# Performance work log

Hardware: AMD Instinct MI355X
Metric: run time of the kernel (lower is better)

The kernel has to match this reference:

```python
import jax, jax.numpy as jnp
import numpy as np

B, TD, TE, H = 8, 128, 256, 512


def setup_inputs() -> dict:
    key = jax.random.key(0)
    k1, k2, k3, k4, k5, k6 = jax.random.split(key, 6)
    enc = jax.random.normal(k1, (B, TE, H), dtype=jnp.float32)
    dec = jax.random.normal(k2, (B, TD, H), dtype=jnp.float32)
    mask = jax.random.randint(k3, (B, TE), 0, 2).astype(jnp.bool_)
    # glorot-ish scale for weights
    W1 = jax.random.normal(k4, (H, H), dtype=jnp.float32) * (1.0 / np.sqrt(H))
    W2 = jax.random.normal(k5, (H, H), dtype=jnp.float32) * (1.0 / np.sqrt(H))
    V = jax.random.normal(k6, (H, 1), dtype=jnp.float32) * (1.0 / np.sqrt(H))
    return {"encoder_outputs": enc, "decoder_outputs": dec,
            "encoder_mask": mask, "W1": W1, "W2": W2, "V": V}


def reference(encoder_outputs, decoder_outputs, encoder_mask, W1, W2, V):
    # Bahdanau additive attention.
    # enc: [B, Te, H], dec: [B, Td, H], mask: [B, Te]
    ew = jnp.einsum('bsh,hk->bsk', encoder_outputs, W1)   # [B, Te, H]
    dw = jnp.einsum('bth,hk->btk', decoder_outputs, W2)   # [B, Td, H]
    # broadcast add -> [B, Td, Te, H] (the large intermediate)
    s = jnp.tanh(ew[:, None, :, :] + dw[:, :, None, :])
    score = jnp.einsum('btsh,h->bts', s, V[:, 0])          # [B, Td, Te]
    m = encoder_mask.astype(jnp.float32)                   # [B, Te]
    score = score + (1.0 - m)[:, None, :] * (-1e9)
    attention_weights = jax.nn.softmax(score, axis=2)      # [B, Td, Te]
    context_vector = jnp.einsum('bts,bsh->bth', attention_weights, encoder_outputs)
    return context_vector, attention_weights
```

## Files before the change

kernel.cpp:

```cpp
#include <hip/hip_runtime.h>
#include <hip/hip_bf16.h>
#include <math.h>

constexpr int kB  = 8;
constexpr int kTD = 128;
constexpr int kTE = 256;
constexpr int kH  = 512;

constexpr float kTwoLog2e = 2.8853900817779268f;
constexpr float kLog2e    = 1.4426950408889634f;

constexpr int TM = 4;
constexpr int GEMM_BLOCKS = 384;

typedef __attribute__((ext_vector_type(8)))  short short8;
typedef __attribute__((ext_vector_type(16))) float f32x16;

__device__ __forceinline__ unsigned short f2bf(float x) {
    unsigned int u = __float_as_uint(x);
    return (unsigned short)((u + 0x7fffu + ((u >> 16) & 1u)) >> 16);
}
__device__ __forceinline__ float bf2f(unsigned short h) {
    return __uint_as_float(((unsigned int)h) << 16);
}

__global__ __launch_bounds__(256)
void prep_kernel(const float* __restrict__ enc, const float* __restrict__ dec,
                 const float* __restrict__ W1, const float* __restrict__ W2,
                 const void* __restrict__ mask_raw,
                 float* __restrict__ ewt, float* __restrict__ dwc,
                 float* __restrict__ mask_f) {
    const int bx = blockIdx.x;
    const int tid = threadIdx.x;

    if (bx == GEMM_BLOCKS) {
        const unsigned int* w = (const unsigned int*)mask_raw;
        unsigned int gt1 = 0, flt = 0;
        for (int i = tid; i < 512; i += 256) {
            unsigned int v = w[i];
            if (v == 0x3f800000u) flt = 1;
            else if (v > 1u) gt1 = 1;
        }
        __shared__ unsigned int s_gt1, s_flt;
        if (tid == 0) { s_gt1 = 0u; s_flt = 0u; }
        __syncthreads();
        if (gt1) atomicOr(&s_gt1, 1u);
        if (flt) atomicOr(&s_flt, 1u);
        __syncthreads();
        const int mode = s_flt ? 2 : (s_gt1 ? 1 : 0);
        for (int i = tid; i < kB * kTE; i += 256) {
            float val;
            if (mode == 2)      val = ((const float*)mask_raw)[i];
            else if (mode == 1) val = (float)(((const unsigned char*)mask_raw)[i]);
            else                val = (float)(((const int*)mask_raw)[i]);
            mask_f[i] = val;
        }
        return;
    }

    const int mt = bx >> 3;
    const int nt = bx & 7;
    const bool is_enc = (mt < 32);
    const int m0 = mt * 64;
    const int n0 = nt * 64;
    const float* Abase = is_enc ? (enc + (size_t)m0 * kH)
                                : (dec + (size_t)(m0 - 2048) * kH);
    const float* W = is_enc ? W1 : W2;

    __shared__ __align__(16) unsigned short Ahi[64][40], Alo[64][40];
    __shared__ __align__(16) unsigned short Bhi[64][40], Blo[64][40];
    __shared__ float Ws[32][68];

    const int lane = tid & 63;
    const int wv   = tid >> 6;
    const int wr   = wv >> 1, wc = wv & 1;
    const int col  = lane & 31, hi5 = lane >> 5;

    const int ar  = tid >> 2;
    const int akc = (tid & 3) * 8;
    const int wkr = tid >> 3;
    const int wnc = (tid & 7) * 8;
    const int pn  = tid & 63;
    const int pkc = (tid >> 6) * 8;

    f32x16 acc = {};

    float4 a0p = *(const float4*)&Abase[(size_t)ar * kH + akc];
    float4 a1p = *(const float4*)&Abase[(size_t)ar * kH + akc + 4];
    float4 w0p = *(const float4*)&W[(size_t)wkr * kH + n0 + wnc];
    float4 w1p = *(const float4*)&W[(size_t)wkr * kH + n0 + wnc + 4];

    for (int step = 0; step < 16; ++step) {
        *(float4*)&Ws[wkr][wnc]     = w0p;
        *(float4*)&Ws[wkr][wnc + 4] = w1p;
        {
            uint4 H, L;
            float f[8] = {a0p.x, a0p.y, a0p.z, a0p.w, a1p.x, a1p.y, a1p.z, a1p.w};
            unsigned short hs[8], ls[8];
            #pragma unroll
            for (int j = 0; j < 8; ++j) {
                hs[j] = f2bf(f[j]);
                ls[j] = f2bf(f[j] - bf2f(hs[j]));
            }
            H.x = hs[0] | (hs[1] << 16); H.y = hs[2] | (hs[3] << 16);
            H.z = hs[4] | (hs[5] << 16); H.w = hs[6] | (hs[7] << 16);
            L.x = ls[0] | (ls[1] << 16); L.y = ls[2] | (ls[3] << 16);
            L.z = ls[4] | (ls[5] << 16); L.w = ls[6] | (ls[7] << 16);
            *(uint4*)&Ahi[ar][akc] = H;
            *(uint4*)&Alo[ar][akc] = L;
        }
        __syncthreads();

        {
            uint4 H, L;
            unsigned short hs[8], ls[8];
            #pragma unroll
            for (int j = 0; j < 8; ++j) {
                float x = Ws[pkc + j][pn];
                hs[j] = f2bf(x);
                ls[j] = f2bf(x - bf2f(hs[j]));
            }
            H.x = hs[0] | (hs[1] << 16); H.y = hs[2] | (hs[3] << 16);
            H.z = hs[4] | (hs[5] << 16); H.w = hs[6] | (hs[7] << 16);
            L.x = ls[0] | (ls[1] << 16); L.y = ls[2] | (ls[3] << 16);
            L.z = ls[4] | (ls[5] << 16); L.w = ls[6] | (ls[7] << 16);
            *(uint4*)&Bhi[pn][pkc] = H;
            *(uint4*)&Blo[pn][pkc] = L;
        }

        if (step < 15) {
            const int k1 = (step + 1) * 32;
            a0p = *(const float4*)&Abase[(size_t)ar * kH + k1 + akc];
            a1p = *(const float4*)&Abase[(size_t)ar * kH + k1 + akc + 4];
            w0p = *(const float4*)&W[(size_t)(k1 + wkr) * kH + n0 + wnc];
            w1p = *(const float4*)&W[(size_t)(k1 + wkr) * kH + n0 + wnc + 4];
        }
        __syncthreads();

        #pragma unroll
        for (int kc = 0; kc < 32; kc += 16) {
            const int ka = kc + hi5 * 8;
            short8 ah = *(const short8*)&Ahi[wr * 32 + col][ka];
            short8 al = *(const short8*)&Alo[wr * 32 + col][ka];
            short8 bh = *(const short8*)&Bhi[wc * 32 + col][ka];
            short8 bl = *(const short8*)&Blo[wc * 32 + col][ka];
            acc = __builtin_amdgcn_mfma_f32_32x32x16_bf16(ah, bh, acc, 0, 0, 0);
            acc = __builtin_amdgcn_mfma_f32_32x32x16_bf16(ah, bl, acc, 0, 0, 0);
            acc = __builtin_amdgcn_mfma_f32_32x32x16_bf16(al, bh, acc, 0, 0, 0);
        }
        __syncthreads();
    }

    const int h = n0 + wc * 32 + col;
    if (is_enc) {
        #pragma unroll
        for (int reg = 0; reg < 16; ++reg) {
            const int row = (reg & 3) + 8 * (reg >> 2) + 4 * hi5;
            const int gm = m0 + wr * 32 + row;
            const int bb = gm >> 8, sE = gm & 255;
            float val = __builtin_amdgcn_exp2f(acc[reg] * kTwoLog2e);
            ewt[(((size_t)bb * 128 + (h >> 2)) * 256 + sE) * 4 + (h & 3)] = val;
        }
    } else {
        #pragma unroll
        for (int reg = 0; reg < 16; ++reg) {
            const int row = (reg & 3) + 8 * (reg >> 2) + 4 * hi5;
            const int dm = (m0 - 2048) + wr * 32 + row;
            float val = __builtin_amdgcn_exp2f(acc[reg] * kTwoLog2e);
            dwc[(size_t)dm * kH + h] = val;
        }
    }
}

__global__ __launch_bounds__(1024, 4)
void fused_attn_kernel(const float* __restrict__ ewt, const float* __restrict__ dwc,
                       const float* __restrict__ enc, const float* __restrict__ V,
                       const float* __restrict__ mask_f,
                       float* __restrict__ ctx_out, float* __restrict__ attn_out) {
    const int bid = blockIdx.x;
    const int b   = bid & 7;
    const int t0  = (bid >> 3) * TM;
    const int tid = threadIdx.x;
    const int s   = tid & 255;
    const int hq  = tid >> 8;
    const int hqu = __builtin_amdgcn_readfirstlane(hq);

    __shared__ float p_s[TM * kH];
    __shared__ float v_s[kH];
    __shared__ union {
        float  part[3 * TM * kTE];
        float4 pctx[4][TM][128];
    } u;
    __shared__ float4 wgt4[kTE];
    __shared__ float red_mx[4][TM], red_sm[4][TM];

    if (tid < 512)
        ((float4*)p_s)[tid] =
            ((const float4*)(dwc + (size_t)(b * kTD + t0) * kH))[tid];
    else if (tid < 640)
        ((float4*)v_s)[tid - 512] = ((const float4*)V)[tid - 512];
    __syncthreads();

    const float4* E4 = (const float4*)ewt + ((size_t)(b * 128 + hqu * 32) * 256 + s);
    const float4* Pq = (const float4*)p_s + hqu * 32;
    const float4* Vq = (const float4*)v_s + hqu * 32;

    float a0 = 0.0f, a1 = 0.0f, a2 = 0.0f, a3 = 0.0f;

#define SCORE_T(eV, gg, qoff, accv)                                        \
    {   float4 q = Pq[(qoff) + (gg)];                                      \
        float A_ = fmaf(eV.x, q.x, 1.0f), B_ = fmaf(eV.y, q.y, 1.0f);      \
        float C_ = fmaf(eV.z, q.z, 1.0f), D_ = fmaf(eV.w, q.w, 1.0f);      \
        float t1 = fmaf(vv.y, A_, vv.x * B_);                              \
        float t2 = fmaf(vv.w, C_, vv.z * D_);                              \
        float AB = A_ * B_, CD = C_ * D_;                                  \
        float num = fmaf(t2, AB, t1 * CD);                                 \
        accv = fmaf(num, __builtin_amdgcn_rcpf(AB * CD), accv); }
#define SCORE_STEP(eV, gg)                                                 \
    {   float4 vv = Vq[gg];                                                \
        SCORE_T(eV, gg, 0, a0)   SCORE_T(eV, gg, 128, a1)                  \
        SCORE_T(eV, gg, 256, a2) SCORE_T(eV, gg, 384, a3) }

    float4 e0 = E4[0];
    float4 e1 = E4[256];
    #pragma unroll 4
    for (int g = 0; g < 32; ++g) {
        const int gp = (g + 2 < 32) ? (g + 2) : 31;
        float4 en = E4[(size_t)gp * 256];
        SCORE_STEP(e0, g)
        e0 = e1; e1 = en;
    }
#undef SCORE_STEP
#undef SCORE_T

    if (hq > 0) {
        float* pp = &u.part[(hq - 1) * TM * kTE];
        pp[0 * kTE + s] = a0; pp[1 * kTE + s] = a1;
        pp[2 * kTE + s] = a2; pp[3 * kTE + s] = a3;
    }
    __syncthreads();

    const bool active = (hq == 0);
    const int wvq = s >> 6;
    float sc0, sc1, sc2, sc3;
    if (active) {
        const float* P = u.part;
        const float pen = (1.0f - mask_f[b * kTE + s]) * -1e9f;
        sc0 = -2.0f * ((a0 + P[0 * TM * kTE + 0 * kTE + s]) +
                       (P[1 * TM * kTE + 0 * kTE + s] + P[2 * TM * kTE + 0 * kTE + s])) + pen;
        sc1 = -2.0f * ((a1 + P[0 * TM * kTE + 1 * kTE + s]) +
                       (P[1 * TM * kTE + 1 * kTE + s] + P[2 * TM * kTE + 1 * kTE + s])) + pen;
        sc2 = -2.0f * ((a2 + P[0 * TM * kTE + 2 * kTE + s]) +
                       (P[1 * TM * kTE + 2 * kTE + s] + P[2 * TM * kTE + 2 * kTE + s])) + pen;
        sc3 = -2.0f * ((a3 + P[0 * TM * kTE + 3 * kTE + s]) +
                       (P[1 * TM * kTE + 3 * kTE + s] + P[2 * TM * kTE + 3 * kTE + s])) + pen;
        float m0 = sc0, m1 = sc1, m2 = sc2, m3 = sc3;
        #pragma unroll
        for (int off = 1; off < 64; off <<= 1) {
            m0 = fmaxf(m0, __shfl_xor(m0, off));
            m1 = fmaxf(m1, __shfl_xor(m1, off));
            m2 = fmaxf(m2, __shfl_xor(m2, off));
            m3 = fmaxf(m3, __shfl_xor(m3, off));
        }
        if ((s & 63) == 0) {
            red_mx[wvq][0] = m0; red_mx[wvq][1] = m1;
            red_mx[wvq][2] = m2; red_mx[wvq][3] = m3;
        }
    }
    __syncthreads();

    float p0, p1, p2, p3;
    if (active) {
        float m0 = fmaxf(fmaxf(red_mx[0][0], red_mx[1][0]), fmaxf(red_mx[2][0], red_mx[3][0]));
        float m1 = fmaxf(fmaxf(red_mx[0][1], red_mx[1][1]), fmaxf(red_mx[2][1], red_mx[3][1]));
        float m2 = fmaxf(fmaxf(red_mx[0][2], red_mx[1][2]), fmaxf(red_mx[2][2], red_mx[3][2]));
        float m3 = fmaxf(fmaxf(red_mx[0][3], red_mx[1][3]), fmaxf(red_mx[2][3], red_mx[3][3]));
        p0 = __builtin_amdgcn_exp2f((sc0 - m0) * kLog2e);
        p1 = __builtin_amdgcn_exp2f((sc1 - m1) * kLog2e);
        p2 = __builtin_amdgcn_exp2f((sc2 - m2) * kLog2e);
        p3 = __builtin_amdgcn_exp2f((sc3 - m3) * kLog2e);
        float s0 = p0, s1 = p1, s2 = p2, s3 = p3;
        #pragma unroll
        for (int off = 1; off < 64; off <<= 1) {
            s0 += __shfl_xor(s0, off);
            s1 += __shfl_xor(s1, off);
            s2 += __shfl_xor(s2, off);
            s3 += __shfl_xor(s3, off);
        }
        if ((s & 63) == 0) {
            red_sm[wvq][0] = s0; red_sm[wvq][1] = s1;
            red_sm[wvq][2] = s2; red_sm[wvq][3] = s3;
        }
    }
    __syncthreads();

    if (active) {
        float s0 = (red_sm[0][0] + red_sm[1][0]) + (red_sm[2][0] + red_sm[3][0]);
        float s1 = (red_sm[0][1] + red_sm[1][1]) + (red_sm[2][1] + red_sm[3][1]);
        float s2 = (red_sm[0][2] + red_sm[1][2]) + (red_sm[2][2] + red_sm[3][2]);
        float s3 = (red_sm[0][3] + red_sm[1][3]) + (red_sm[2][3] + red_sm[3][3]);
        float4 w;
        w.x = p0 * __builtin_amdgcn_rcpf(s0);
        w.y = p1 * __builtin_amdgcn_rcpf(s1);
        w.z = p2 * __builtin_amdgcn_rcpf(s2);
        w.w = p3 * __builtin_amdgcn_rcpf(s3);
        wgt4[s] = w;
        float* ao = attn_out + (size_t)(b * kTD + t0) * kTE + s;
        ao[0]       = w.x;
        ao[kTE]     = w.y;
        ao[2 * kTE] = w.z;
        ao[3 * kTE] = w.w;
    }
    __syncthreads();

    const int th4 = tid & 127;
    const int sq  = tid >> 7;
    const float4* enc4 = (const float4*)(enc + (size_t)b * kTE * kH);
    float4 c[TM];
    #pragma unroll
    for (int t = 0; t < TM; ++t) c[t] = float4{0.f, 0.f, 0.f, 0.f};
    #pragma unroll 4
    for (int i = 0; i < 32; ++i) {
        const int ss = sq * 32 + i;
        float4 e = enc4[(size_t)ss * 128 + th4];
        float4 w = wgt4[ss];
        c[0].x = fmaf(w.x, e.x, c[0].x); c[0].y = fmaf(w.x, e.y, c[0].y);
        c[0].z = fmaf(w.x, e.z, c[0].z); c[0].w = fmaf(w.x, e.w, c[0].w);
        c[1].x = fmaf(w.y, e.x, c[1].x); c[1].y = fmaf(w.y, e.y, c[1].y);
        c[1].z = fmaf(w.y, e.z, c[1].z); c[1].w = fmaf(w.y, e.w, c[1].w);
        c[2].x = fmaf(w.z, e.x, c[2].x); c[2].y = fmaf(w.z, e.y, c[2].y);
        c[2].z = fmaf(w.z, e.z, c[2].z); c[2].w = fmaf(w.z, e.w, c[2].w);
        c[3].x = fmaf(w.w, e.x, c[3].x); c[3].y = fmaf(w.w, e.y, c[3].y);
        c[3].z = fmaf(w.w, e.z, c[3].z); c[3].w = fmaf(w.w, e.w, c[3].w);
    }
    if (sq >= 4) {
        #pragma unroll
        for (int t = 0; t < TM; ++t) u.pctx[sq - 4][t][th4] = c[t];
    }
    __syncthreads();
    if (sq < 4) {
        #pragma unroll
        for (int t = 0; t < TM; ++t) {
            float4 p = u.pctx[sq][t][th4];
            c[t].x += p.x; c[t].y += p.y; c[t].z += p.z; c[t].w += p.w;
        }
    }
    __syncthreads();
    if (sq >= 1 && sq < 4) {
        #pragma unroll
        for (int t = 0; t < TM; ++t) u.pctx[sq - 1][t][th4] = c[t];
    }
    __syncthreads();
    if (sq == 0) {
        #pragma unroll
        for (int t = 0; t < TM; ++t) {
            float4 q0v = u.pctx[0][t][th4];
            float4 q1v = u.pctx[1][t][th4];
            float4 q2v = u.pctx[2][t][th4];
            c[t].x += (q0v.x + q1v.x) + q2v.x;
            c[t].y += (q0v.y + q1v.y) + q2v.y;
            c[t].z += (q0v.z + q1v.z) + q2v.z;
            c[t].w += (q0v.w + q1v.w) + q2v.w;
            *(float4*)&ctx_out[(size_t)(b * kTD + t0 + t) * kH + th4 * 4] = c[t];
        }
    }
}

extern "C" void kernel_launch(void* const* d_in, const int* in_sizes, int n_in,
                              void* d_out, int out_size, void* d_ws, size_t ws_size,
                              hipStream_t stream) {
    const float* enc  = (const float*)d_in[0];
    const float* dec  = (const float*)d_in[1];
    const void*  mask = d_in[2];
    const float* W1   = (const float*)d_in[3];
    const float* W2   = (const float*)d_in[4];
    const float* V    = (const float*)d_in[5];

    float* ctx_out  = (float*)d_out;
    float* attn_out = (float*)d_out + kB * kTD * kH;

    char* ws = (char*)d_ws;
    float* mask_f = (float*)ws;
    float* ewt    = (float*)(ws + 8192);
    float* dwc    = (float*)(ws + 8192 + (size_t)kB * kTE * kH * 4);

    hipLaunchKernelGGL(prep_kernel, dim3(GEMM_BLOCKS + 1), dim3(256), 0, stream,
                       enc, dec, W1, W2, mask, ewt, dwc, mask_f);
    hipLaunchKernelGGL(fused_attn_kernel, dim3(kB * kTD / TM), dim3(1024), 0, stream,
                       ewt, dwc, enc, V, mask_f, ctx_out, attn_out);
}
```

Baseline: 45.60 us.

## Split score reduction across waves by hidden slice with tree reduction and single-wave softmax

Reassigns score work so each wave handles a slice of the hidden dimension for all encoder positions, reusing decoder and V values across four positions per lane. Partial scores are combined with a shared-memory tree reduction, after which wave 0 performs the softmax using only wave shuffles. This removes the cross-wave softmax reductions but adds more barriers, more LDS, and higher register pressure, and serializes the softmax onto a single wave.

```diff
diff --git a/kernel.cpp b/kernel.cpp
--- a/kernel.cpp
+++ b/kernel.cpp
@@ -177,22 +177,20 @@
                        const float* __restrict__ enc, const float* __restrict__ V,
                        const float* __restrict__ mask_f,
                        float* __restrict__ ctx_out, float* __restrict__ attn_out) {
-    const int bid = blockIdx.x;
-    const int b   = bid & 7;
-    const int t0  = (bid >> 3) * TM;
-    const int tid = threadIdx.x;
-    const int s   = tid & 255;
-    const int hq  = tid >> 8;
-    const int hqu = __builtin_amdgcn_readfirstlane(hq);
+    const int bid  = blockIdx.x;
+    const int b    = bid & 7;
+    const int t0   = (bid >> 3) * TM;
+    const int tid  = threadIdx.x;
+    const int lane = tid & 63;
+    const int w    = tid >> 6;
 
     __shared__ float p_s[TM * kH];
     __shared__ float v_s[kH];
     __shared__ union {
-        float  part[3 * TM * kTE];
+        float  F[8 * 1024];
         float4 pctx[4][TM][128];
     } u;
     __shared__ float4 wgt4[kTE];
-    __shared__ float red_mx[4][TM], red_sm[4][TM];
 
     if (tid < 512)
         ((float4*)p_s)[tid] =
@@ -201,115 +199,107 @@
         ((float4*)v_s)[tid - 512] = ((const float4*)V)[tid - 512];
     __syncthreads();
 
-    const float4* E4 = (const float4*)ewt + ((size_t)(b * 128 + hqu * 32) * 256 + s);
-    const float4* Pq = (const float4*)p_s + hqu * 32;
-    const float4* Vq = (const float4*)v_s + hqu * 32;
-
-    float a0 = 0.0f, a1 = 0.0f, a2 = 0.0f, a3 = 0.0f;
-
-#define SCORE_T(eV, gg, qoff, accv)                                        \
-    {   float4 q = Pq[(qoff) + (gg)];                                      \
-        float A_ = fmaf(eV.x, q.x, 1.0f), B_ = fmaf(eV.y, q.y, 1.0f);      \
-        float C_ = fmaf(eV.z, q.z, 1.0f), D_ = fmaf(eV.w, q.w, 1.0f);      \
+    const float4* E4b = (const float4*)ewt + (size_t)(b * 128 + w * 8) * 256;
+    const float4* Pq  = (const float4*)p_s;
+    const float4* Vq  = (const float4*)v_s;
+
+    float acc00=0.f, acc01=0.f, acc02=0.f, acc03=0.f;
+    float acc10=0.f, acc11=0.f, acc12=0.f, acc13=0.f;
+    float acc20=0.f, acc21=0.f, acc22=0.f, acc23=0.f;
+    float acc30=0.f, acc31=0.f, acc32=0.f, acc33=0.f;
+
+#define SCORE_T(eV, qV, accv)                                              \
+    {   float A_ = fmaf(eV.x, qV.x, 1.0f), B_ = fmaf(eV.y, qV.y, 1.0f);    \
+        float C_ = fmaf(eV.z, qV.z, 1.0f), D_ = fmaf(eV.w, qV.w, 1.0f);    \
         float t1 = fmaf(vv.y, A_, vv.x * B_);                              \
         float t2 = fmaf(vv.w, C_, vv.z * D_);                              \
         float AB = A_ * B_, CD = C_ * D_;                                  \
         float num = fmaf(t2, AB, t1 * CD);                                 \
         accv = fmaf(num, __builtin_amdgcn_rcpf(AB * CD), accv); }
-#define SCORE_STEP(eV, gg)                                                 \
-    {   float4 vv = Vq[gg];                                                \
-        SCORE_T(eV, gg, 0, a0)   SCORE_T(eV, gg, 128, a1)                  \
-        SCORE_T(eV, gg, 256, a2) SCORE_T(eV, gg, 384, a3) }
-
-    float4 e0 = E4[0];
-    float4 e1 = E4[256];
-    #pragma unroll 4
-    for (int g = 0; g < 32; ++g) {
-        const int gp = (g + 2 < 32) ? (g + 2) : 31;
-        float4 en = E4[(size_t)gp * 256];
-        SCORE_STEP(e0, g)
-        e0 = e1; e1 = en;
-    }
-#undef SCORE_STEP
+#define SCORE_J(jj)                                                        \
+    {   float4 e = E4b[(size_t)hg * 256 + lane + 64 * (jj)];               \
+        SCORE_T(e, q0, acc##jj##0) SCORE_T(e, q1, acc##jj##1)              \
+        SCORE_T(e, q2, acc##jj##2) SCORE_T(e, q3, acc##jj##3) }
+
+    #pragma unroll 2
+    for (int hg = 0; hg < 8; ++hg) {
+        const int h4 = w * 8 + hg;
+        float4 vv = Vq[h4];
+        float4 q0 = Pq[0 * 128 + h4];
+        float4 q1 = Pq[1 * 128 + h4];
+        float4 q2 = Pq[2 * 128 + h4];
+        float4 q3 = Pq[3 * 128 + h4];
+        SCORE_J(0) SCORE_J(1) SCORE_J(2) SCORE_J(3)
+    }
+#undef SCORE_J
 #undef SCORE_T
 
-    if (hq > 0) {
-        float* pp = &u.part[(hq - 1) * TM * kTE];
-        pp[0 * kTE + s] = a0; pp[1 * kTE + s] = a1;
-        pp[2 * kTE + s] = a2; pp[3 * kTE + s] = a3;
-    }
-    __syncthreads();
-
-    const bool active = (hq == 0);
-    const int wvq = s >> 6;
-    float sc0, sc1, sc2, sc3;
-    if (active) {
-        const float* P = u.part;
-        const float pen = (1.0f - mask_f[b * kTE + s]) * -1e9f;
-        sc0 = -2.0f * ((a0 + P[0 * TM * kTE + 0 * kTE + s]) +
-                       (P[1 * TM * kTE + 0 * kTE + s] + P[2 * TM * kTE + 0 * kTE + s])) + pen;
-        sc1 = -2.0f * ((a1 + P[0 * TM * kTE + 1 * kTE + s]) +
-                       (P[1 * TM * kTE + 1 * kTE + s] + P[2 * TM * kTE + 1 * kTE + s])) + pen;
-        sc2 = -2.0f * ((a2 + P[0 * TM * kTE + 2 * kTE + s]) +
-                       (P[1 * TM * kTE + 2 * kTE + s] + P[2 * TM * kTE + 2 * kTE + s])) + pen;
-        sc3 = -2.0f * ((a3 + P[0 * TM * kTE + 3 * kTE + s]) +
-                       (P[1 * TM * kTE + 3 * kTE + s] + P[2 * TM * kTE + 3 * kTE + s])) + pen;
-        float m0 = sc0, m1 = sc1, m2 = sc2, m3 = sc3;
-        #pragma unroll
-        for (int off = 1; off < 64; off <<= 1) {
-            m0 = fmaxf(m0, __shfl_xor(m0, off));
-            m1 = fmaxf(m1, __shfl_xor(m1, off));
-            m2 = fmaxf(m2, __shfl_xor(m2, off));
-            m3 = fmaxf(m3, __shfl_xor(m3, off));
-        }
-        if ((s & 63) == 0) {
-            red_mx[wvq][0] = m0; red_mx[wvq][1] = m1;
-            red_mx[wvq][2] = m2; red_mx[wvq][3] = m3;
-        }
-    }
-    __syncthreads();
-
-    float p0, p1, p2, p3;
-    if (active) {
-        float m0 = fmaxf(fmaxf(red_mx[0][0], red_mx[1][0]), fmaxf(red_mx[2][0], red_mx[3][0]));
-        float m1 = fmaxf(fmaxf(red_mx[0][1], red_mx[1][1]), fmaxf(red_mx[2][1], red_mx[3][1]));
-        float m2 = fmaxf(fmaxf(red_mx[0][2], red_mx[1][2]), fmaxf(red_mx[2][2], red_mx[3][2]));
-        float m3 = fmaxf(fmaxf(red_mx[0][3], red_mx[1][3]), fmaxf(red_mx[2][3], red_mx[3][3]));
-        p0 = __builtin_amdgcn_exp2f((sc0 - m0) * kLog2e);
-        p1 = __builtin_amdgcn_exp2f((sc1 - m1) * kLog2e);
-        p2 = __builtin_amdgcn_exp2f((sc2 - m2) * kLog2e);
-        p3 = __builtin_amdgcn_exp2f((sc3 - m3) * kLog2e);
-        float s0 = p0, s1 = p1, s2 = p2, s3 = p3;
-        #pragma unroll
-        for (int off = 1; off < 64; off <<= 1) {
-            s0 += __shfl_xor(s0, off);
-            s1 += __shfl_xor(s1, off);
-            s2 += __shfl_xor(s2, off);
-            s3 += __shfl_xor(s3, off);
-        }
-        if ((s & 63) == 0) {
-            red_sm[wvq][0] = s0; red_sm[wvq][1] = s1;
-            red_sm[wvq][2] = s2; red_sm[wvq][3] = s3;
-        }
-    }
-    __syncthreads();
-
-    if (active) {
-        float s0 = (red_sm[0][0] + red_sm[1][0]) + (red_sm[2][0] + red_sm[3][0]);
-        float s1 = (red_sm[0][1] + red_sm[1][1]) + (red_sm[2][1] + red_sm[3][1]);
-        float s2 = (red_sm[0][2] + red_sm[1][2]) + (red_sm[2][2] + red_sm[3][2]);
-        float s3 = (red_sm[0][3] + red_sm[1][3]) + (red_sm[2][3] + red_sm[3][3]);
-        float4 w;
-        w.x = p0 * __builtin_amdgcn_rcpf(s0);
-        w.y = p1 * __builtin_amdgcn_rcpf(s1);
-        w.z = p2 * __builtin_amdgcn_rcpf(s2);
-        w.w = p3 * __builtin_amdgcn_rcpf(s3);
-        wgt4[s] = w;
-        float* ao = attn_out + (size_t)(b * kTD + t0) * kTE + s;
-        ao[0]       = w.x;
-        ao[kTE]     = w.y;
-        ao[2 * kTE] = w.z;
-        ao[3 * kTE] = w.w;
+#define WRITE_ACC(dst)                                                     \
+    {   dst[0*64]=acc00;  dst[1*64]=acc01;  dst[2*64]=acc02;  dst[3*64]=acc03;  \
+        dst[4*64]=acc10;  dst[5*64]=acc11;  dst[6*64]=acc12;  dst[7*64]=acc13;  \
+        dst[8*64]=acc20;  dst[9*64]=acc21;  dst[10*64]=acc22; dst[11*64]=acc23; \
+        dst[12*64]=acc30; dst[13*64]=acc31; dst[14*64]=acc32; dst[15*64]=acc33; }
+#define READ_ACC(src)                                                      \
+    {   acc00+=src[0*64];  acc01+=src[1*64];  acc02+=src[2*64];  acc03+=src[3*64];  \
+        acc10+=src[4*64];  acc11+=src[5*64];  acc12+=src[6*64];  acc13+=src[7*64];  \
+        acc20+=src[8*64];  acc21+=src[9*64];  acc22+=src[10*64]; acc23+=src[11*64]; \
+        acc30+=src[12*64]; acc31+=src[13*64]; acc32+=src[14*64]; acc33+=src[15*64]; }
+
+    #pragma unroll
+    for (int size = 16; size > 1; size >>= 1) {
+        const int half = size >> 1;
+        if (w >= half && w < size) {
+            float* dst = u.F + (size_t)(w - half) * 1024 + lane;
+            WRITE_ACC(dst)
+        }
+        __syncthreads();
+        if (w < half) {
+            const float* src = u.F + (size_t)w * 1024 + lane;
+            READ_ACC(src)
+        }
+        __syncthreads();
+    }
+#undef WRITE_ACC
+#undef READ_ACC
+
+    if (w == 0) {
+        float pen0 = (1.0f - mask_f[b * kTE + lane +   0]) * -1e9f;
+        float pen1 = (1.0f - mask_f[b * kTE + lane +  64]) * -1e9f;
+        float pen2 = (1.0f - mask_f[b * kTE + lane + 128]) * -1e9f;
+        float pen3 = (1.0f - mask_f[b * kTE + lane + 192]) * -1e9f;
+        float sc[4][4];
+        sc[0][0] = fmaf(-2.f, acc00, pen0); sc[0][1] = fmaf(-2.f, acc10, pen1);
+        sc[0][2] = fmaf(-2.f, acc20, pen2); sc[0][3] = fmaf(-2.f, acc30, pen3);
+        sc[1][0] = fmaf(-2.f, acc01, pen0); sc[1][1] = fmaf(-2.f, acc11, pen1);
+        sc[1][2] = fmaf(-2.f, acc21, pen2); sc[1][3] = fmaf(-2.f, acc31, pen3);
+        sc[2][0] = fmaf(-2.f, acc02, pen0); sc[2][1] = fmaf(-2.f, acc12, pen1);
+        sc[2][2] = fmaf(-2.f, acc22, pen2); sc[2][3] = fmaf(-2.f, acc32, pen3);
+        sc[3][0] = fmaf(-2.f, acc03, pen0); sc[3][1] = fmaf(-2.f, acc13, pen1);
+        sc[3][2] = fmaf(-2.f, acc23, pen2); sc[3][3] = fmaf(-2.f, acc33, pen3);
+
+        #pragma unroll
+        for (int t = 0; t < 4; ++t) {
+            float m = fmaxf(fmaxf(sc[t][0], sc[t][1]), fmaxf(sc[t][2], sc[t][3]));
+            #pragma unroll
+            for (int off = 1; off < 64; off <<= 1)
+                m = fmaxf(m, __shfl_xor(m, off));
+            float pj0 = __builtin_amdgcn_exp2f((sc[t][0] - m) * kLog2e);
+            float pj1 = __builtin_amdgcn_exp2f((sc[t][1] - m) * kLog2e);
+            float pj2 = __builtin_amdgcn_exp2f((sc[t][2] - m) * kLog2e);
+            float pj3 = __builtin_amdgcn_exp2f((sc[t][3] - m) * kLog2e);
+            float ssum = (pj0 + pj1) + (pj2 + pj3);
+            #pragma unroll
+            for (int off = 1; off < 64; off <<= 1)
+                ssum += __shfl_xor(ssum, off);
+            const float inv = __builtin_amdgcn_rcpf(ssum);
+            float* wf = (float*)wgt4;
+            float* ao = attn_out + (size_t)(b * kTD + t0 + t) * kTE;
+            float g0 = pj0 * inv, g1 = pj1 * inv, g2 = pj2 * inv, g3 = pj3 * inv;
+            wf[(lane +   0) * 4 + t] = g0;  ao[lane +   0] = g0;
+            wf[(lane +  64) * 4 + t] = g1;  ao[lane +  64] = g1;
+            wf[(lane + 128) * 4 + t] = g2;  ao[lane + 128] = g2;
+            wf[(lane + 192) * 4 + t] = g3;  ao[lane + 192] = g3;
+        }
     }
     __syncthreads();
 
@@ -323,15 +313,15 @@
     for (int i = 0; i < 32; ++i) {
         const int ss = sq * 32 + i;
         float4 e = enc4[(size_t)ss * 128 + th4];
-        float4 w = wgt4[ss];
-        c[0].x = fmaf(w.x, e.x, c[0].x); c[0].y = fmaf(w.x, e.y, c[0].y);
-        c[0].z = fmaf(w.x, e.z, c[0].z); c[0].w = fmaf(w.x, e.w, c[0].w);
-        c[1].x = fmaf(w.y, e.x, c[1].x); c[1].y = fmaf(w.y, e.y, c[1].y);
-        c[1].z = fmaf(w.y, e.z, c[1].z); c[1].w = fmaf(w.y, e.w, c[1].w);
-        c[2].x = fmaf(w.z, e.x, c[2].x); c[2].y = fmaf(w.z, e.y, c[2].y);
-        c[2].z = fmaf(w.z, e.z, c[2].z); c[2].w = fmaf(w.z, e.w, c[2].w);
-        c[3].x = fmaf(w.w, e.x, c[3].x); c[3].y = fmaf(w.w, e.y, c[3].y);
-        c[3].z = fmaf(w.w, e.z, c[3].z); c[3].w = fmaf(w.w, e.w, c[3].w);
+        float4 wv = wgt4[ss];
+        c[0].x = fmaf(wv.x, e.x, c[0].x); c[0].y = fmaf(wv.x, e.y, c[0].y);
+        c[0].z = fmaf(wv.x, e.z, c[0].z); c[0].w = fmaf(wv.x, e.w, c[0].w);
+        c[1].x = fmaf(wv.y, e.x, c[1].x); c[1].y = fmaf(wv.y, e.y, c[1].y);
+        c[1].z = fmaf(wv.y, e.z, c[1].z); c[1].w = fmaf(wv.y, e.w, c[1].w);
+        c[2].x = fmaf(wv.z, e.x, c[2].x); c[2].y = fmaf(wv.z, e.y, c[2].y);
+        c[2].z = fmaf(wv.z, e.z, c[2].z); c[2].w = fmaf(wv.z, e.w, c[2].w);
+        c[3].x = fmaf(wv.w, e.x, c[3].x); c[3].y = fmaf(wv.w, e.y, c[3].y);
+        c[3].z = fmaf(wv.w, e.z, c[3].z); c[3].w = fmaf(wv.w, e.w, c[3].w);
     }
     if (sq >= 4) {
         #pragma unroll
```

Result: no change. 44.77 us (-1.8%).
